# Optimization experiments

Measured on AMD Instinct MI355X. Metric: run time of the kernel, lower is better.

## Reference

```python
import jax, jax.numpy as jnp
import numpy as np

N = 40000
E = 640000
D_IN = 128
H = 8
C = 16  # out_dim per head


def setup_inputs() -> dict:
    key = jax.random.key(0)
    ks = jax.random.split(key, 7)
    features = jax.random.normal(ks[0], (N, D_IN), dtype=jnp.float32)
    edge_index = jax.random.randint(ks[1], (2, E), 0, N, dtype=jnp.int32)
    edge_weight = jax.random.uniform(ks[2], (E,), dtype=jnp.float32)
    # xavier-ish scales
    W_lin = jax.random.normal(ks[3], (D_IN, H * C), dtype=jnp.float32) * (1.0 / np.sqrt(D_IN))
    att_l = jax.random.normal(ks[4], (1, H, C), dtype=jnp.float32) * 0.1
    att_r = jax.random.normal(ks[5], (1, H, C), dtype=jnp.float32) * 0.1
    W_res = jax.random.normal(ks[6], (D_IN, H * C), dtype=jnp.float32) * (1.0 / np.sqrt(D_IN))
    return {"features": features, "edge_index": edge_index, "edge_weight": edge_weight,
            "W_lin": W_lin, "att_l": att_l, "att_r": att_r, "W_res": W_res}


def _segment_softmax(logits, seg, num_segments):
    # logits: (E, H), seg: (E,) destination node ids
    m = jax.ops.segment_max(logits, seg, num_segments=num_segments)  # (N, H)
    ex = jnp.exp(logits - m[seg])
    s = jax.ops.segment_sum(ex, seg, num_segments=num_segments)  # (N, H)
    return ex / s[seg]


def reference(features, edge_index, edge_weight, W_lin, att_l, att_r, W_res):
    src, dst = edge_index[0], edge_index[1]
    x = (features @ W_lin).reshape(-1, H, C)              # (N, H, C)
    alpha_l = (x * att_l).sum(-1)                          # (N, H)
    alpha_r = (x * att_r).sum(-1)                          # (N, H)
    alpha = alpha_l[src] + alpha_r[dst]                    # (E, H)
    alpha = edge_weight[:, None] * alpha
    alpha = jnp.where(alpha >= 0, alpha, 0.2 * alpha)      # leaky_relu(0.2)
    coef = _segment_softmax(alpha, dst, N)                 # (E, H)
    msgs = x[src] * coef[:, :, None]                       # (E, H, C)
    agg = jax.ops.segment_sum(msgs, dst, num_segments=N)   # (N, H, C)
    out = jax.nn.elu(agg).reshape(-1, H * C)
    out = out + features @ W_res
    return out
```

## Files before the change

### kernel.cpp

```cpp
#include <hip/hip_runtime.h>
#include <math.h>

#define N_NODES 40000
#define N_EDGES 640000
#define D 128
#define H 8
#define C 16
#define NBG 1250
#define KP 136
#define NBUCK 625
#define NCH 512
#define ECH 1250
#define MAXB 1536

typedef __attribute__((ext_vector_type(8))) short short8;
typedef __attribute__((ext_vector_type(4))) float floatx4;


__device__ __forceinline__ unsigned short f2bf(float f) {
  const unsigned u = __float_as_uint(f);
  return (unsigned short)((u + 0x7FFFu + ((u >> 16) & 1u)) >> 16);
}
__device__ __forceinline__ float bflo(unsigned p) {
  return __uint_as_float(p << 16);
}
__device__ __forceinline__ float bfhi(unsigned p) {
  return __uint_as_float(p & 0xFFFF0000u);
}
__device__ __forceinline__ float bf2f(unsigned short u) {
  return __uint_as_float((unsigned)u << 16);
}

__global__ void k_prep(const float* __restrict__ Wlin,
                       const float* __restrict__ Wres,
                       unsigned short* __restrict__ wt)
{
  const int n = blockIdx.x, k = threadIdx.x, g = blockIdx.y;
  const float* W = g ? Wres : Wlin;
  wt[((g * 128 + n) * 128) + k] = f2bf(W[(long)k * 128 + n]);
}

__global__ __launch_bounds__(256, 4) void k_gemm(
    const float* __restrict__ feat, const unsigned short* __restrict__ wt,
    unsigned short* __restrict__ xh, float* __restrict__ outp,
    const float* __restrict__ attl, const float* __restrict__ attr,
    float* __restrict__ al, float* __restrict__ ar)
{
  __shared__ short sA[32 * KP];
  __shared__ float sD[32 * 132];
  const int t = threadIdx.x;
  const int row0 = blockIdx.x * 32;

  {
    const int kq = t & 31;
    const int rb = (t >> 5) * 4;
    #pragma unroll
    for (int i = 0; i < 4; ++i) {
      const int r = rb + i;
      const float4 f = *(const float4*)&feat[(long)(row0 + r) * 128 + kq * 4];
      const unsigned lo = (unsigned)f2bf(f.x) | ((unsigned)f2bf(f.y) << 16);
      const unsigned hi = (unsigned)f2bf(f.z) | ((unsigned)f2bf(f.w) << 16);
      *(uint2*)&sA[r * KP + kq * 4] = make_uint2(lo, hi);
    }
  }

  const int w = t >> 6, lane = t & 63;
  const int c15 = lane & 15, q = lane >> 4;

  short8 bfr0[4][2], bfr1[4][2];
  #pragma unroll
  for (int kc = 0; kc < 4; ++kc)
    #pragma unroll
    for (int nt = 0; nt < 2; ++nt) {
      const int n = (w * 2 + nt) * 16 + c15;
      bfr0[kc][nt] = *(const short8*)&wt[n * 128 + kc * 32 + q * 8];
      bfr1[kc][nt] = *(const short8*)&wt[16384 + n * 128 + kc * 32 + q * 8];
    }
  __syncthreads();

  floatx4 acc0[2][2], acc1[2][2];
  #pragma unroll
  for (int mt = 0; mt < 2; ++mt)
    #pragma unroll
    for (int nt = 0; nt < 2; ++nt) {
      acc0[mt][nt] = (floatx4){0.f, 0.f, 0.f, 0.f};
      acc1[mt][nt] = (floatx4){0.f, 0.f, 0.f, 0.f};
    }
  #pragma unroll
  for (int kc = 0; kc < 4; ++kc)
    #pragma unroll
    for (int mt = 0; mt < 2; ++mt) {
      const short8 afr = *(const short8*)&sA[(mt * 16 + c15) * KP + kc * 32 + q * 8];
      acc0[mt][0] = __builtin_amdgcn_mfma_f32_16x16x32_bf16(afr, bfr0[kc][0], acc0[mt][0], 0, 0, 0);
      acc0[mt][1] = __builtin_amdgcn_mfma_f32_16x16x32_bf16(afr, bfr0[kc][1], acc0[mt][1], 0, 0, 0);
      acc1[mt][0] = __builtin_amdgcn_mfma_f32_16x16x32_bf16(afr, bfr1[kc][0], acc1[mt][0], 0, 0, 0);
      acc1[mt][1] = __builtin_amdgcn_mfma_f32_16x16x32_bf16(afr, bfr1[kc][1], acc1[mt][1], 0, 0, 0);
    }

  const int orow = t >> 3, seg = t & 7;
  const int grow = row0 + orow;

  #pragma unroll
  for (int mt = 0; mt < 2; ++mt)
    #pragma unroll
    for (int nt = 0; nt < 2; ++nt) {
      const int col = (w * 2 + nt) * 16 + c15;
      #pragma unroll
      for (int r = 0; r < 4; ++r)
        sD[(mt * 16 + q * 4 + r) * 132 + col] = acc0[mt][nt][r];
    }
  __syncthreads();
  {
    #pragma unroll
    for (int i = 0; i < 2; ++i) {
      const float4 v0 = *(const float4*)&sD[orow * 132 + seg * 16 + i * 8];
      const float4 v1 = *(const float4*)&sD[orow * 132 + seg * 16 + i * 8 + 4];
      uint4 u;
      u.x = (unsigned)f2bf(v0.x) | ((unsigned)f2bf(v0.y) << 16);
      u.y = (unsigned)f2bf(v0.z) | ((unsigned)f2bf(v0.w) << 16);
      u.z = (unsigned)f2bf(v1.x) | ((unsigned)f2bf(v1.y) << 16);
      u.w = (unsigned)f2bf(v1.z) | ((unsigned)f2bf(v1.w) << 16);
      *(uint4*)&xh[(long)grow * 128 + seg * 16 + i * 8] = u;
    }
    const int h = seg;
    float sl = 0.f, sr = 0.f;
    #pragma unroll
    for (int c4 = 0; c4 < 4; ++c4) {
      const float4 xv = *(const float4*)&sD[orow * 132 + h * 16 + c4 * 4];
      const float4 lv = *(const float4*)&attl[h * 16 + c4 * 4];
      const float4 rv = *(const float4*)&attr[h * 16 + c4 * 4];
      sl += xv.x * lv.x + xv.y * lv.y + xv.z * lv.z + xv.w * lv.w;
      sr += xv.x * rv.x + xv.y * rv.y + xv.z * rv.z + xv.w * rv.w;
    }
    al[(long)grow * 8 + h] = sl;
    ar[(long)grow * 8 + h] = sr;
  }
  __syncthreads();

  #pragma unroll
  for (int mt = 0; mt < 2; ++mt)
    #pragma unroll
    for (int nt = 0; nt < 2; ++nt) {
      const int col = (w * 2 + nt) * 16 + c15;
      #pragma unroll
      for (int r = 0; r < 4; ++r)
        sD[(mt * 16 + q * 4 + r) * 132 + col] = acc1[mt][nt][r];
    }
  __syncthreads();
  #pragma unroll
  for (int i = 0; i < 4; ++i) {
    const float4 v = *(const float4*)&sD[orow * 132 + seg * 16 + i * 4];
    *(float4*)&outp[(long)grow * 128 + seg * 16 + i * 4] = v;
  }
}

__global__ __launch_bounds__(512) void k_cnt(
    const int* __restrict__ dst, int* __restrict__ rank, int* __restrict__ cnt2)
{
  __shared__ int lcnt[NBUCK];
  const int t = threadIdx.x;
  const int c = blockIdx.x;
  for (int i = t; i < NBUCK; i += 512) lcnt[i] = 0;
  __syncthreads();
  const int e0 = c * ECH;
  for (int e = e0 + t; e < e0 + ECH; e += 512)
    rank[e] = atomicAdd(&lcnt[dst[e] >> 6], 1);
  __syncthreads();
  for (int i = t; i < NBUCK; i += 512) cnt2[c * NBUCK + i] = lcnt[i];
}

__global__ __launch_bounds__(512) void k_scan2a(
    const int* __restrict__ cnt2, int* __restrict__ pre2T, int* __restrict__ total)
{
  __shared__ int sd[NCH];
  const int b = blockIdx.x;
  const int t = threadIdx.x;
  const int v = cnt2[t * NBUCK + b];
  sd[t] = v;
  __syncthreads();
  #pragma unroll
  for (int off = 1; off < NCH; off <<= 1) {
    const int add = (t >= off) ? sd[t - off] : 0;
    __syncthreads();
    sd[t] += add;
    __syncthreads();
  }
  pre2T[b * NCH + t] = sd[t] - v;
  if (t == NCH - 1) total[b] = sd[t];
}

__global__ __launch_bounds__(1024) void k_scan_g(
    const int* __restrict__ total, int* __restrict__ gbase)
{
  __shared__ int sd[1024];
  const int t = threadIdx.x;
  const int v = (t < NBUCK) ? total[t] : 0;
  sd[t] = v;
  __syncthreads();
  #pragma unroll
  for (int off = 1; off < 1024; off <<= 1) {
    const int add = (t >= off) ? sd[t - off] : 0;
    __syncthreads();
    sd[t] += add;
    __syncthreads();
  }
  if (t < NBUCK) gbase[t] = sd[t] - v;
}

__global__ __launch_bounds__(256) void k_fill(
    const int* __restrict__ src, const int* __restrict__ dst,
    const float* __restrict__ ew, const float* __restrict__ al,
    const float* __restrict__ ar, const int* __restrict__ gbase,
    const int* __restrict__ pre2T, const int* __restrict__ rank,
    unsigned short* __restrict__ pexph, int* __restrict__ meta)
{
  const int e = blockIdx.x * 256 + threadIdx.x;
  if (e >= N_EDGES) return;
  const int s = src[e], d = dst[e];
  const float w = ew[e];
  const int b = d >> 6;
  const int c = e / ECH;
  const int p = gbase[b] + pre2T[b * NCH + c] + rank[e];
  const float4 l0 = *(const float4*)&al[(long)s * 8];
  const float4 l1 = *(const float4*)&al[(long)s * 8 + 4];
  const float4 r0 = *(const float4*)&ar[(long)d * 8];
  const float4 r1 = *(const float4*)&ar[(long)d * 8 + 4];
  float lv[8] = {l0.x + r0.x, l0.y + r0.y, l0.z + r0.z, l0.w + r0.w,
                 l1.x + r1.x, l1.y + r1.y, l1.z + r1.z, l1.w + r1.w};
  #pragma unroll
  for (int h = 0; h < 8; ++h) {
    float a = w * lv[h];
    a = (a >= 0.f) ? a : 0.2f * a;
    lv[h] = __expf(a);
  }
  meta[p] = ((d & 63) << 16) | s;
  uint4 u;
  u.x = (unsigned)f2bf(lv[0]) | ((unsigned)f2bf(lv[1]) << 16);
  u.y = (unsigned)f2bf(lv[2]) | ((unsigned)f2bf(lv[3]) << 16);
  u.z = (unsigned)f2bf(lv[4]) | ((unsigned)f2bf(lv[5]) << 16);
  u.w = (unsigned)f2bf(lv[6]) | ((unsigned)f2bf(lv[7]) << 16);
  *(uint4*)&pexph[(long)p * 8] = u;
}

__global__ __launch_bounds__(256) void k_sort(
    const int* __restrict__ gbase, const int* __restrict__ total,
    int* __restrict__ meta, unsigned short* __restrict__ pexph,
    int* __restrict__ nodeS)
{
  __shared__ int sm_raw[MAXB];
  __shared__ uint4 sm_pex[MAXB];
  __shared__ int bcnt[64], bbase[64], bpos[64];
  const int b = blockIdx.x;
  const int start = gbase[b];
  const int cntb = total[b];
  const int t = threadIdx.x;
  if (t < 64) bcnt[t] = 0;
  __syncthreads();
  for (int i = t; i < cntb; i += 256) {
    const int m = meta[start + i];
    sm_raw[i] = m;
    sm_pex[i] = *(const uint4*)&pexph[(long)(start + i) * 8];
    atomicAdd(&bcnt[m >> 16], 1);
  }
  __syncthreads();
  if (t < 64) {
    const int v = bcnt[t];
    int incl = v;
    #pragma unroll
    for (int off = 1; off < 64; off <<= 1) {
      const int n = __shfl_up(incl, off, 64);
      if (t >= off) incl += n;
    }
    bbase[t] = incl - v;
    bpos[t] = 0;
    nodeS[(b << 6) + t] = start + incl - v;
  }
  if (b == 0 && t == 64) nodeS[N_NODES] = N_EDGES;
  __syncthreads();
  for (int i = t; i < cntb; i += 256) {
    const int m = sm_raw[i];
    const int dl = m >> 16;
    const int r = atomicAdd(&bpos[dl], 1);
    const int q = start + bbase[dl] + r;
    meta[q] = m & 0xFFFF;
    *(uint4*)&pexph[(long)q * 8] = sm_pex[i];
  }
}

__global__ __launch_bounds__(256) void k_node_agg(
    const int* __restrict__ nodeS, const int* __restrict__ psrc,
    const unsigned short* __restrict__ pexph,
    const unsigned short* __restrict__ xh, float* __restrict__ outp)
{
  const int wave = threadIdx.x >> 6;
  const int lane = threadIdx.x & 63;
  const int d = blockIdx.x * 4 + wave;
  const int start = nodeS[d];
  const int end = nodeS[d + 1];
  if (end <= start) return;

  const int h = lane >> 3;
  const int co = lane * 2;

  float2 a0 = {0.f, 0.f}, a1 = {0.f, 0.f}, a2 = {0.f, 0.f}, a3 = {0.f, 0.f};
  float s0s = 0.f, s1s = 0.f, s2s = 0.f, s3s = 0.f;
  int p = start;
  for (; p + 4 <= end; p += 4) {
    const int s0 = psrc[p + 0], s1 = psrc[p + 1];
    const int s2 = psrc[p + 2], s3 = psrc[p + 3];
    const float e0 = bf2f(pexph[(long)(p + 0) * 8 + h]);
    const float e1 = bf2f(pexph[(long)(p + 1) * 8 + h]);
    const float e2 = bf2f(pexph[(long)(p + 2) * 8 + h]);
    const float e3 = bf2f(pexph[(long)(p + 3) * 8 + h]);
    const unsigned v0 = *(const unsigned*)&xh[(long)s0 * 128 + co];
    const unsigned v1 = *(const unsigned*)&xh[(long)s1 * 128 + co];
    const unsigned v2 = *(const unsigned*)&xh[(long)s2 * 128 + co];
    const unsigned v3 = *(const unsigned*)&xh[(long)s3 * 128 + co];
    a0.x = fmaf(bflo(v0), e0, a0.x); a0.y = fmaf(bfhi(v0), e0, a0.y); s0s += e0;
    a1.x = fmaf(bflo(v1), e1, a1.x); a1.y = fmaf(bfhi(v1), e1, a1.y); s1s += e1;
    a2.x = fmaf(bflo(v2), e2, a2.x); a2.y = fmaf(bfhi(v2), e2, a2.y); s2s += e2;
    a3.x = fmaf(bflo(v3), e3, a3.x); a3.y = fmaf(bfhi(v3), e3, a3.y); s3s += e3;
  }
  for (; p < end; ++p) {
    const int s = psrc[p];
    const float e0 = bf2f(pexph[(long)p * 8 + h]);
    const unsigned v = *(const unsigned*)&xh[(long)s * 128 + co];
    a0.x = fmaf(bflo(v), e0, a0.x);
    a0.y = fmaf(bfhi(v), e0, a0.y);
    s0s += e0;
  }
  const float rs = 1.0f / ((s0s + s1s) + (s2s + s3s));
  const float ax = ((a0.x + a1.x) + (a2.x + a3.x)) * rs;
  const float ay = ((a0.y + a1.y) + (a2.y + a3.y)) * rs;

  float2 o = *(float2*)&outp[(long)d * 128 + co];
  o.x += (ax > 0.f) ? ax : expm1f(ax);
  o.y += (ay > 0.f) ? ay : expm1f(ay);
  *(float2*)&outp[(long)d * 128 + co] = o;
}

extern "C" void kernel_launch(void* const* d_in, const int* in_sizes, int n_in,
                              void* d_out, int out_size, void* d_ws, size_t ws_size,
                              hipStream_t stream) {
  const float* feat = (const float*)d_in[0];
  const int*   eidx = (const int*)d_in[1];
  const float* ew   = (const float*)d_in[2];
  const float* Wlin = (const float*)d_in[3];
  const float* attl = (const float*)d_in[4];
  const float* attr = (const float*)d_in[5];
  const float* Wres = (const float*)d_in[6];
  float* outp = (float*)d_out;

  float* ws = (float*)d_ws;
  unsigned short* xh = (unsigned short*)ws;
  float* al   = ws + 5120000;
  float* ar   = ws + 5440000;
  unsigned short* pexph = (unsigned short*)(ws + 5760000);
  int*   rank = (int*)(ws + 8320000);
  int*   meta = (int*)(ws + 10880000);
  int*   cnt2 = (int*)(ws + 11560000);
  int*   pre2T = (int*)(ws + 11880000);
  int*   total = (int*)(ws + 12200000);
  int*   gbase = (int*)(ws + 12210000);
  int*   nodeS = (int*)(ws + 12220000);
  unsigned short* wt = (unsigned short*)(ws + 12800000);

  const int* src = eidx;
  const int* dst = eidx + N_EDGES;

  dim3 pgrid(128, 2);
  k_prep<<<pgrid, 128, 0, stream>>>(Wlin, Wres, wt);
  k_gemm<<<NBG, 256, 0, stream>>>(feat, wt, xh, outp, attl, attr, al, ar);
  k_cnt<<<NCH, 512, 0, stream>>>(dst, rank, cnt2);
  k_scan2a<<<NBUCK, NCH, 0, stream>>>(cnt2, pre2T, total);
  k_scan_g<<<1, 1024, 0, stream>>>(total, gbase);
  k_fill<<<(N_EDGES + 255) / 256, 256, 0, stream>>>(src, dst, ew, al, ar,
                                                    gbase, pre2T, rank,
                                                    pexph, meta);
  k_sort<<<NBUCK, 256, 0, stream>>>(gbase, total, meta, pexph, nodeS);
  k_node_agg<<<N_NODES / 4, 256, 0, stream>>>(nodeS, meta, pexph, xh, outp);
}
```

Baseline: 183.6 us.

## Fuse edge bucketing count into GEMM grid and move edge logits into sort

The destination-bucket counting kernel is folded into the GEMM launch as a second grid row, so counting runs alongside the GEMM blocks. Each edge's bucket, local node and rank are packed into one int. The fill kernel now scatters only a compact (src|dl, weight) record, and the attention logits and exp are computed inside the per-bucket sort kernel, using a shared-memory copy of the bucket's ar values. This cuts the scattered 16-byte pexph traffic, which was previously written and then rewritten, and drops the per-edge ar gathers, in exchange for extra ALU work in the sort kernel and a larger GEMM grid.

```diff
diff --git a/kernel.cpp b/kernel.cpp
--- a/kernel.cpp
+++ b/kernel.cpp
@@ -44,11 +44,29 @@
     const float* __restrict__ feat, const unsigned short* __restrict__ wt,
     unsigned short* __restrict__ xh, float* __restrict__ outp,
     const float* __restrict__ attl, const float* __restrict__ attr,
-    float* __restrict__ al, float* __restrict__ ar)
+    float* __restrict__ al, float* __restrict__ ar,
+    const int* __restrict__ dst, int* __restrict__ pk, int* __restrict__ cnt2)
 {
   __shared__ short sA[32 * KP];
   __shared__ float sD[32 * 132];
   const int t = threadIdx.x;
+
+  if (blockIdx.y == 1) {
+    if (blockIdx.x >= NCH) return;
+    int* lcnt = (int*)sA;
+    for (int i = t; i < NBUCK; i += 256) lcnt[i] = 0;
+    __syncthreads();
+    const int c = blockIdx.x, e0 = c * ECH;
+    for (int e = e0 + t; e < e0 + ECH; e += 256) {
+      const int d = dst[e];
+      const int r = atomicAdd(&lcnt[d >> 6], 1);
+      pk[e] = ((d >> 6) << 17) | ((d & 63) << 11) | r;
+    }
+    __syncthreads();
+    for (int i = t; i < NBUCK; i += 256) cnt2[c * NBUCK + i] = lcnt[i];
+    return;
+  }
+
   const int row0 = blockIdx.x * 32;
 
   {
@@ -154,21 +172,6 @@
   }
 }
 
-__global__ __launch_bounds__(512) void k_cnt(
-    const int* __restrict__ dst, int* __restrict__ rank, int* __restrict__ cnt2)
-{
-  __shared__ int lcnt[NBUCK];
-  const int t = threadIdx.x;
-  const int c = blockIdx.x;
-  for (int i = t; i < NBUCK; i += 512) lcnt[i] = 0;
-  __syncthreads();
-  const int e0 = c * ECH;
-  for (int e = e0 + t; e < e0 + ECH; e += 512)
-    rank[e] = atomicAdd(&lcnt[dst[e] >> 6], 1);
-  __syncthreads();
-  for (int i = t; i < NBUCK; i += 512) cnt2[c * NBUCK + i] = lcnt[i];
-}
-
 __global__ __launch_bounds__(512) void k_scan2a(
     const int* __restrict__ cnt2, int* __restrict__ pre2T, int* __restrict__ total)
 {
@@ -207,60 +210,42 @@
   if (t < NBUCK) gbase[t] = sd[t] - v;
 }
 
-__global__ __launch_bounds__(256) void k_fill(
-    const int* __restrict__ src, const int* __restrict__ dst,
-    const float* __restrict__ ew, const float* __restrict__ al,
-    const float* __restrict__ ar, const int* __restrict__ gbase,
-    const int* __restrict__ pre2T, const int* __restrict__ rank,
-    unsigned short* __restrict__ pexph, int* __restrict__ meta)
+__global__ __launch_bounds__(256) void k_place(
+    const int* __restrict__ pk, const int* __restrict__ src,
+    const float* __restrict__ ew, const int* __restrict__ gbase,
+    const int* __restrict__ pre2T, uint2* __restrict__ einfo)
 {
   const int e = blockIdx.x * 256 + threadIdx.x;
   if (e >= N_EDGES) return;
-  const int s = src[e], d = dst[e];
-  const float w = ew[e];
-  const int b = d >> 6;
+  const int k = pk[e];
+  const int b = k >> 17, dl = (k >> 11) & 63, r = k & 2047;
   const int c = e / ECH;
-  const int p = gbase[b] + pre2T[b * NCH + c] + rank[e];
-  const float4 l0 = *(const float4*)&al[(long)s * 8];
-  const float4 l1 = *(const float4*)&al[(long)s * 8 + 4];
-  const float4 r0 = *(const float4*)&ar[(long)d * 8];
-  const float4 r1 = *(const float4*)&ar[(long)d * 8 + 4];
-  float lv[8] = {l0.x + r0.x, l0.y + r0.y, l0.z + r0.z, l0.w + r0.w,
-                 l1.x + r1.x, l1.y + r1.y, l1.z + r1.z, l1.w + r1.w};
-  #pragma unroll
-  for (int h = 0; h < 8; ++h) {
-    float a = w * lv[h];
-    a = (a >= 0.f) ? a : 0.2f * a;
-    lv[h] = __expf(a);
-  }
-  meta[p] = ((d & 63) << 16) | s;
-  uint4 u;
-  u.x = (unsigned)f2bf(lv[0]) | ((unsigned)f2bf(lv[1]) << 16);
-  u.y = (unsigned)f2bf(lv[2]) | ((unsigned)f2bf(lv[3]) << 16);
-  u.z = (unsigned)f2bf(lv[4]) | ((unsigned)f2bf(lv[5]) << 16);
-  u.w = (unsigned)f2bf(lv[6]) | ((unsigned)f2bf(lv[7]) << 16);
-  *(uint4*)&pexph[(long)p * 8] = u;
-}
-
-__global__ __launch_bounds__(256) void k_sort(
+  const int p = gbase[b] + pre2T[b * NCH + c] + r;
+  einfo[p] = make_uint2(((unsigned)src[e] << 6) | (unsigned)dl,
+                        __float_as_uint(ew[e]));
+}
+
+__global__ __launch_bounds__(256) void k_edge(
     const int* __restrict__ gbase, const int* __restrict__ total,
-    int* __restrict__ meta, unsigned short* __restrict__ pexph,
+    const uint2* __restrict__ einfo, const float* __restrict__ al,
+    const float* __restrict__ ar,
+    unsigned short* __restrict__ pexph, int* __restrict__ psrc,
     int* __restrict__ nodeS)
 {
-  __shared__ int sm_raw[MAXB];
-  __shared__ uint4 sm_pex[MAXB];
+  __shared__ uint2 sE[MAXB];
+  __shared__ float sAr[512];
   __shared__ int bcnt[64], bbase[64], bpos[64];
   const int b = blockIdx.x;
   const int start = gbase[b];
   const int cntb = total[b];
   const int t = threadIdx.x;
   if (t < 64) bcnt[t] = 0;
+  for (int i = t; i < 512; i += 256) sAr[i] = ar[((long)b << 6) * 8 + i];
   __syncthreads();
   for (int i = t; i < cntb; i += 256) {
-    const int m = meta[start + i];
-    sm_raw[i] = m;
-    sm_pex[i] = *(const uint4*)&pexph[(long)(start + i) * 8];
-    atomicAdd(&bcnt[m >> 16], 1);
+    const uint2 m = einfo[start + i];
+    sE[i] = m;
+    atomicAdd(&bcnt[m.x & 63], 1);
   }
   __syncthreads();
   if (t < 64) {
@@ -278,12 +263,30 @@
   if (b == 0 && t == 64) nodeS[N_NODES] = N_EDGES;
   __syncthreads();
   for (int i = t; i < cntb; i += 256) {
-    const int m = sm_raw[i];
-    const int dl = m >> 16;
+    const uint2 m = sE[i];
+    const int dl = m.x & 63;
+    const int s = (int)(m.x >> 6);
+    const float w = __uint_as_float(m.y);
+    const float4 l0 = *(const float4*)&al[(long)s * 8];
+    const float4 l1 = *(const float4*)&al[(long)s * 8 + 4];
+    const float* arr = &sAr[dl * 8];
+    float lv[8] = {l0.x + arr[0], l0.y + arr[1], l0.z + arr[2], l0.w + arr[3],
+                   l1.x + arr[4], l1.y + arr[5], l1.z + arr[6], l1.w + arr[7]};
+    #pragma unroll
+    for (int h = 0; h < 8; ++h) {
+      float a = w * lv[h];
+      a = (a >= 0.f) ? a : 0.2f * a;
+      lv[h] = __expf(a);
+    }
     const int r = atomicAdd(&bpos[dl], 1);
     const int q = start + bbase[dl] + r;
-    meta[q] = m & 0xFFFF;
-    *(uint4*)&pexph[(long)q * 8] = sm_pex[i];
+    psrc[q] = s;
+    uint4 u;
+    u.x = (unsigned)f2bf(lv[0]) | ((unsigned)f2bf(lv[1]) << 16);
+    u.y = (unsigned)f2bf(lv[2]) | ((unsigned)f2bf(lv[3]) << 16);
+    u.z = (unsigned)f2bf(lv[4]) | ((unsigned)f2bf(lv[5]) << 16);
+    u.w = (unsigned)f2bf(lv[6]) | ((unsigned)f2bf(lv[7]) << 16);
+    *(uint4*)&pexph[(long)q * 8] = u;
   }
 }
 
@@ -356,8 +359,9 @@
   float* al   = ws + 5120000;
   float* ar   = ws + 5440000;
   unsigned short* pexph = (unsigned short*)(ws + 5760000);
-  int*   rank = (int*)(ws + 8320000);
-  int*   meta = (int*)(ws + 10880000);
+  int*   pk   = (int*)(ws + 8320000);
+  uint2* einfo = (uint2*)(ws + 9000000);
+  int*   psrc = (int*)(ws + 10880000);
   int*   cnt2 = (int*)(ws + 11560000);
   int*   pre2T = (int*)(ws + 11880000);
   int*   total = (int*)(ws + 12200000);
@@ -370,13 +374,14 @@
 
   dim3 pgrid(128, 2);
   k_prep<<<pgrid, 128, 0, stream>>>(Wlin, Wres, wt);
-  k_gemm<<<NBG, 256, 0, stream>>>(feat, wt, xh, outp, attl, attr, al, ar);
-  k_cnt<<<NCH, 512, 0, stream>>>(dst, rank, cnt2);
+  dim3 ggrid(NBG, 2);
+  k_gemm<<<ggrid, 256, 0, stream>>>(feat, wt, xh, outp, attl, attr, al, ar,
+                                    dst, pk, cnt2);
   k_scan2a<<<NBUCK, NCH, 0, stream>>>(cnt2, pre2T, total);
   k_scan_g<<<1, 1024, 0, stream>>>(total, gbase);
-  k_fill<<<(N_EDGES + 255) / 256, 256, 0, stream>>>(src, dst, ew, al, ar,
-                                                    gbase, pre2T, rank,
-                                                    pexph, meta);
-  k_sort<<<NBUCK, 256, 0, stream>>>(gbase, total, meta, pexph, nodeS);
-  k_node_agg<<<N_NODES / 4, 256, 0, stream>>>(nodeS, meta, pexph, xh, outp);
-}
+  k_place<<<(N_EDGES + 255) / 256, 256, 0, stream>>>(pk, src, ew, gbase,
+                                                     pre2T, einfo);
+  k_edge<<<NBUCK, 256, 0, stream>>>(gbase, total, einfo, al, ar,
+                                    pexph, psrc, nodeS);
+  k_node_agg<<<N_NODES / 4, 256, 0, stream>>>(nodeS, psrc, pexph, xh, outp);
+}
```

Measured after the change: 164.0 us. 1.12x faster.
